# Kernel tuning notes

Measured on AMD Instinct MI355X. Metric: run time of the kernel, lower is better.

Reference implementation:

```python
import jax, jax.numpy as jnp
import numpy as np

B, H, S, D = 2, 16, 2048, 64

def setup_inputs() -> dict:
    key = jax.random.key(0)
    kq, kk, kv = jax.random.split(key, 3)
    Q = jax.random.normal(kq, (B, H, S, D), dtype=jnp.float32)
    K = jax.random.normal(kk, (B, H, S, D), dtype=jnp.float32)
    V = jax.random.normal(kv, (B, H, S, D), dtype=jnp.float32)
    return {"Q": Q, "K": K, "V": V}

def reference(Q, K, V):
    # scores: [B, H, S, S]
    scale = 1.0 / jnp.sqrt(jnp.asarray(Q.shape[-1], Q.dtype))
    scores = jnp.einsum('bhqd,bhkd->bhqk', Q, K) * scale
    probs = jax.nn.softmax(scores, axis=-1)
    out = jnp.einsum('bhqk,bhkd->bhqd', probs, V)
    return out
```

## Files before the change

kernel.cpp:

```cpp
#include <hip/hip_runtime.h>
#include <hip/hip_bf16.h>


#define Bn 2
#define Hn 16
#define Sn 2048
#define Dn 64
#define KP 72
#define OP 68

typedef __attribute__((ext_vector_type(8)))  short s16x8;
typedef __attribute__((ext_vector_type(16))) float f32x16;

__device__ __forceinline__ float fast_exp2(float x) {
#if __has_builtin(__builtin_amdgcn_exp2f)
    return __builtin_amdgcn_exp2f(x);
#else
    return exp2f(x);
#endif
}
__device__ __forceinline__ unsigned short f2bf(float f) {
    unsigned u = __float_as_uint(f);
    return (unsigned short)((u + 0x7fffu + ((u >> 16) & 1u)) >> 16);
}
__device__ __forceinline__ unsigned pack2bf(float lo, float hi) {
    return (unsigned)f2bf(lo) | ((unsigned)f2bf(hi) << 16);
}
__device__ __forceinline__ unsigned packtrunc(float lo, float hi) {
#if __has_builtin(__builtin_amdgcn_perm)
    return __builtin_amdgcn_perm(__float_as_uint(hi), __float_as_uint(lo),
                                 0x07060302u);
#else
    return (__float_as_uint(lo) >> 16) | (__float_as_uint(hi) & 0xffff0000u);
#endif
}
__device__ __forceinline__ s16x8 lds_frag(const unsigned short* p) {
    uint4 u = *(const uint4*)p;
    return __builtin_bit_cast(s16x8, u);
}
__device__ __forceinline__ s16x8 reg_frag(uint4 u) {
    return __builtin_bit_cast(s16x8, u);
}

__global__ __launch_bounds__(256)
void cast_kv2(const float* __restrict__ K, const float* __restrict__ V,
              unsigned short* __restrict__ Kb, unsigned short* __restrict__ Vt) {
    __shared__ unsigned short TK[64 * 72];
    __shared__ unsigned short TV[64 * 72];
    const int tid = threadIdx.x;
    const int bh  = blockIdx.x >> 5;
    const int kt  = blockIdx.x & 31;
    const int r = tid >> 2, cc = (tid & 3) * 16;

    const size_t rowbase = ((size_t)bh * Sn + (size_t)kt * 64 + r) * Dn + cc;
    {
        const float* ks = K + rowbase;
        #pragma unroll
        for (int i = 0; i < 2; ++i) {
            float4 f0 = *(const float4*)(ks + 8 * i);
            float4 f1 = *(const float4*)(ks + 8 * i + 4);
            uint4 w;
            w.x = pack2bf(f0.x, f0.y); w.y = pack2bf(f0.z, f0.w);
            w.z = pack2bf(f1.x, f1.y); w.w = pack2bf(f1.z, f1.w);
            *(uint4*)(TK + r * 72 + cc + 8 * i) = w;
        }
    }
    {
        const float* vs = V + rowbase;
        #pragma unroll
        for (int i = 0; i < 4; ++i) {
            float4 f = *(const float4*)(vs + 4 * i);
            const int d0 = cc + 4 * i;
            TV[(d0 + 0) * 72 + r] = f2bf(f.x);
            TV[(d0 + 1) * 72 + r] = f2bf(f.y);
            TV[(d0 + 2) * 72 + r] = f2bf(f.z);
            TV[(d0 + 3) * 72 + r] = f2bf(f.w);
        }
    }
    __syncthreads();
    unsigned short* kd = Kb + ((size_t)(bh * 32 + kt) * 8) * 512;
    unsigned short* vd = Vt + ((size_t)(bh * 32 + kt) * 8) * 512;
    #pragma unroll
    for (int i = 0; i < 2; ++i) {
        const int u = i * 256 + tid;
        const int c = u >> 6, lane = u & 63;
        const int l31 = lane & 31, hf = lane >> 5;
        const int sub = c >> 2, ks = c & 3;
        const int off = (sub * 32 + l31) * 72 + ks * 16 + hf * 8;
        *(uint4*)(kd + c * 512 + lane * 8) = *(const uint4*)(TK + off);
        *(uint4*)(vd + c * 512 + lane * 8) = *(const uint4*)(TV + off);
    }
}

__global__ __launch_bounds__(256, 4)
void attn_fwd_mfma5(const float* __restrict__ Q,
                    const unsigned short* __restrict__ Kb,
                    const unsigned short* __restrict__ Vt,
                    float* __restrict__ O) {
    __shared__ __align__(16) char smem[18432];
    unsigned short* PT = (unsigned short*)smem;
    float* ob = (float*)smem;
    float* lb = ob + 64 * OP;

    const int tid  = threadIdx.x;
    const int wave = tid >> 6;
    const int lane = tid & 63;
    const int l31  = lane & 31;
    const int half = lane >> 5;
    const int qg   = wave & 1;
    const int kh   = wave >> 1;

    const int bh = blockIdx.x & 31;
    const int q0 = (blockIdx.x >> 5) * 64;

    const float FCT = 0.18033688011112042f;

    s16x8 qf[4];
    {
        const float* qp = Q + ((size_t)bh * Sn + q0 + qg * 32 + l31) * Dn;
        #pragma unroll
        for (int ks = 0; ks < 4; ++ks) {
            const int d0 = ks * 16 + half * 8;
            float4 f0 = *(const float4*)(qp + d0);
            float4 f1 = *(const float4*)(qp + d0 + 4);
            uint4 u;
            u.x = pack2bf(f0.x * FCT, f0.y * FCT);
            u.y = pack2bf(f0.z * FCT, f0.w * FCT);
            u.z = pack2bf(f1.x * FCT, f1.y * FCT);
            u.w = pack2bf(f1.z * FCT, f1.w * FCT);
            qf[ks] = __builtin_bit_cast(s16x8, u);
        }
    }

    f32x16 acc0, acc1;
    #pragma unroll
    for (int r = 0; r < 16; ++r) { acc0[r] = 0.f; acc1[r] = 0.f; }
    float l = 0.f;

    const unsigned short* kbase =
        Kb + ((size_t)(bh * 32 + kh * 16) * 8) * 512 + (size_t)lane * 8;
    const unsigned short* vbase =
        Vt + ((size_t)(bh * 32 + kh * 16) * 8) * 512 + (size_t)lane * 8;

    unsigned short* ptw = PT + ((size_t)wave * 32 + l31) * KP;

    #pragma unroll 1
    for (int t = 0; t < 16; ++t) {
        uint4 kk[8];
        #pragma unroll
        for (int c = 0; c < 8; ++c)
            kk[c] = *(const uint4*)(kbase + (size_t)(t * 8 + c) * 512);

        f32x16 c0, c1;
        #pragma unroll
        for (int r = 0; r < 16; ++r) { c0[r] = 0.f; c1[r] = 0.f; }
        #pragma unroll
        for (int ks = 0; ks < 4; ++ks) {
            c0 = __builtin_amdgcn_mfma_f32_32x32x16_bf16(reg_frag(kk[ks]),     qf[ks], c0, 0, 0, 0);
            c1 = __builtin_amdgcn_mfma_f32_32x32x16_bf16(reg_frag(kk[4 + ks]), qf[ks], c1, 0, 0, 0);
        }

        uint4 vv[8];
        #pragma unroll
        for (int c = 0; c < 8; ++c)
            vv[c] = *(const uint4*)(vbase + (size_t)(t * 8 + c) * 512);

        #pragma unroll
        for (int r = 0; r < 16; ++r) {
            c0[r] = fast_exp2(c0[r]);
            c1[r] = fast_exp2(c1[r]);
        }
        float a0 = 0.f, a1 = 0.f, a2 = 0.f, a3 = 0.f;
        #pragma unroll
        for (int r = 0; r < 16; r += 4) {
            a0 += c0[r]     + c1[r];
            a1 += c0[r + 1] + c1[r + 1];
            a2 += c0[r + 2] + c1[r + 2];
            a3 += c0[r + 3] + c1[r + 3];
        }
        l += (a0 + a1) + (a2 + a3);

        #pragma unroll
        for (int g = 0; g < 4; ++g) {
            uint2 w0, w1;
            w0.x = packtrunc(c0[4 * g + 0], c0[4 * g + 1]);
            w0.y = packtrunc(c0[4 * g + 2], c0[4 * g + 3]);
            w1.x = packtrunc(c1[4 * g + 0], c1[4 * g + 1]);
            w1.y = packtrunc(c1[4 * g + 2], c1[4 * g + 3]);
            *(uint2*)(ptw + 8 * g + 4 * half)      = w0;
            *(uint2*)(ptw + 8 * g + 4 * half + 32) = w1;
        }

        #pragma unroll
        for (int ks = 0; ks < 4; ++ks) {
            s16x8 pf = lds_frag(ptw + ks * 16 + half * 8);
            acc0 = __builtin_amdgcn_mfma_f32_32x32x16_bf16(reg_frag(vv[ks]),     pf, acc0, 0, 0, 0);
            acc1 = __builtin_amdgcn_mfma_f32_32x32x16_bf16(reg_frag(vv[4 + ks]), pf, acc1, 0, 0, 0);
        }
    }

    l += __shfl_xor(l, 32, 64);

    __syncthreads();
    const int qrow = qg * 32 + l31;
    if (kh == 0) {
        #pragma unroll
        for (int g = 0; g < 4; ++g) {
            const int d0 = 8 * g + 4 * half;
            float4 f;
            f.x = acc0[4*g+0]; f.y = acc0[4*g+1]; f.z = acc0[4*g+2]; f.w = acc0[4*g+3];
            *(float4*)(ob + qrow * OP + d0) = f;
            f.x = acc1[4*g+0]; f.y = acc1[4*g+1]; f.z = acc1[4*g+2]; f.w = acc1[4*g+3];
            *(float4*)(ob + qrow * OP + d0 + 32) = f;
        }
        if (half == 0) lb[qrow] = l;
    }
    __syncthreads();
    if (kh == 1) {
        const float inv = 1.0f / (l + lb[qrow]);
        #pragma unroll
        for (int g = 0; g < 4; ++g) {
            const int d0 = 8 * g + 4 * half;
            float* p;
            float4 f;
            p = ob + qrow * OP + d0;        f = *(float4*)p;
            f.x = (f.x + acc0[4*g+0]) * inv; f.y = (f.y + acc0[4*g+1]) * inv;
            f.z = (f.z + acc0[4*g+2]) * inv; f.w = (f.w + acc0[4*g+3]) * inv;
            *(float4*)p = f;
            p = ob + qrow * OP + d0 + 32;   f = *(float4*)p;
            f.x = (f.x + acc1[4*g+0]) * inv; f.y = (f.y + acc1[4*g+1]) * inv;
            f.z = (f.z + acc1[4*g+2]) * inv; f.w = (f.w + acc1[4*g+3]) * inv;
            *(float4*)p = f;
        }
    }
    __syncthreads();
    float* op = O + ((size_t)bh * Sn + q0) * Dn;
    #pragma unroll
    for (int it = 0; it < 4; ++it) {
        const int idx = it * 256 + tid;
        const int r = idx >> 4, c4 = (idx & 15) * 4;
        *(float4*)(op + r * Dn + c4) = *(float4*)(ob + r * OP + c4);
    }
}

extern "C" void kernel_launch(void* const* d_in, const int* in_sizes, int n_in,
                              void* d_out, int out_size, void* d_ws, size_t ws_size,
                              hipStream_t stream) {
    const float* Q = (const float*)d_in[0];
    const float* K = (const float*)d_in[1];
    const float* V = (const float*)d_in[2];
    float* O = (float*)d_out;

    const size_t elems = (size_t)Bn * Hn * Sn * Dn;
    unsigned short* Kb = (unsigned short*)d_ws;
    unsigned short* Vt = Kb + elems;

    cast_kv2<<<dim3(Bn * Hn * (Sn / 64)), dim3(256), 0, stream>>>(K, V, Kb, Vt);
    attn_fwd_mfma5<<<dim3(Bn * Hn * (Sn / 64)), dim3(256), 0, stream>>>(Q, Kb, Vt, O);
}
```

Before: 139.8 us.

## Split key range four ways per block with 32-query tiles

Each block now handles 32 queries instead of 64, and all four waves share the same query rows while each takes a quarter of the key sequence. Partial outputs and row sums are merged serially through shared memory over several barriers. The grid doubles in size and launch bounds rise to allow more resident blocks, aiming for better CU fill and latency hiding. In exchange, each K/V tile is loaded by twice as many blocks, which doubles global/L2 traffic, and the reduction adds synchronization.

```diff
diff --git a/kernel.cpp b/kernel.cpp
--- a/kernel.cpp
+++ b/kernel.cpp
@@ -92,32 +92,30 @@
     }
 }
 
-__global__ __launch_bounds__(256, 4)
-void attn_fwd_mfma5(const float* __restrict__ Q,
+__global__ __launch_bounds__(256, 5)
+void attn_fwd_mfma6(const float* __restrict__ Q,
                     const unsigned short* __restrict__ Kb,
                     const unsigned short* __restrict__ Vt,
                     float* __restrict__ O) {
     __shared__ __align__(16) char smem[18432];
     unsigned short* PT = (unsigned short*)smem;
     float* ob = (float*)smem;
-    float* lb = ob + 64 * OP;
+    float* lb = ob + 32 * OP;
 
     const int tid  = threadIdx.x;
     const int wave = tid >> 6;
     const int lane = tid & 63;
     const int l31  = lane & 31;
     const int half = lane >> 5;
-    const int qg   = wave & 1;
-    const int kh   = wave >> 1;
 
     const int bh = blockIdx.x & 31;
-    const int q0 = (blockIdx.x >> 5) * 64;
+    const int q0 = (blockIdx.x >> 5) * 32;
 
     const float FCT = 0.18033688011112042f;
 
     s16x8 qf[4];
     {
-        const float* qp = Q + ((size_t)bh * Sn + q0 + qg * 32 + l31) * Dn;
+        const float* qp = Q + ((size_t)bh * Sn + q0 + l31) * Dn;
         #pragma unroll
         for (int ks = 0; ks < 4; ++ks) {
             const int d0 = ks * 16 + half * 8;
@@ -138,14 +136,14 @@
     float l = 0.f;
 
     const unsigned short* kbase =
-        Kb + ((size_t)(bh * 32 + kh * 16) * 8) * 512 + (size_t)lane * 8;
+        Kb + ((size_t)(bh * 32 + wave * 8) * 8) * 512 + (size_t)lane * 8;
     const unsigned short* vbase =
-        Vt + ((size_t)(bh * 32 + kh * 16) * 8) * 512 + (size_t)lane * 8;
+        Vt + ((size_t)(bh * 32 + wave * 8) * 8) * 512 + (size_t)lane * 8;
 
     unsigned short* ptw = PT + ((size_t)wave * 32 + l31) * KP;
 
     #pragma unroll 1
-    for (int t = 0; t < 16; ++t) {
+    for (int t = 0; t < 8; ++t) {
         uint4 kk[8];
         #pragma unroll
         for (int c = 0; c < 8; ++c)
@@ -202,32 +200,56 @@
     l += __shfl_xor(l, 32, 64);
 
     __syncthreads();
-    const int qrow = qg * 32 + l31;
-    if (kh == 0) {
+    if (wave == 0) {
         #pragma unroll
         for (int g = 0; g < 4; ++g) {
             const int d0 = 8 * g + 4 * half;
             float4 f;
             f.x = acc0[4*g+0]; f.y = acc0[4*g+1]; f.z = acc0[4*g+2]; f.w = acc0[4*g+3];
-            *(float4*)(ob + qrow * OP + d0) = f;
+            *(float4*)(ob + l31 * OP + d0) = f;
             f.x = acc1[4*g+0]; f.y = acc1[4*g+1]; f.z = acc1[4*g+2]; f.w = acc1[4*g+3];
-            *(float4*)(ob + qrow * OP + d0 + 32) = f;
-        }
-        if (half == 0) lb[qrow] = l;
-    }
-    __syncthreads();
-    if (kh == 1) {
-        const float inv = 1.0f / (l + lb[qrow]);
+            *(float4*)(ob + l31 * OP + d0 + 32) = f;
+        }
+        if (half == 0) lb[l31] = l;
+    }
+    __syncthreads();
+    if (wave == 1 || wave == 2) {
+        for (int w = 1; w <= 2; ++w) {
+            if (wave == w) {
+                #pragma unroll
+                for (int g = 0; g < 4; ++g) {
+                    const int d0 = 8 * g + 4 * half;
+                    float4 f;
+                    float* p;
+                    p = ob + l31 * OP + d0;       f = *(float4*)p;
+                    f.x += acc0[4*g+0]; f.y += acc0[4*g+1];
+                    f.z += acc0[4*g+2]; f.w += acc0[4*g+3];
+                    *(float4*)p = f;
+                    p = ob + l31 * OP + d0 + 32;  f = *(float4*)p;
+                    f.x += acc1[4*g+0]; f.y += acc1[4*g+1];
+                    f.z += acc1[4*g+2]; f.w += acc1[4*g+3];
+                    *(float4*)p = f;
+                }
+                if (half == 0) lb[l31] += l;
+            }
+            __syncthreads();
+        }
+    } else {
+        __syncthreads();
+        __syncthreads();
+    }
+    if (wave == 3) {
+        const float inv = 1.0f / (l + lb[l31]);
         #pragma unroll
         for (int g = 0; g < 4; ++g) {
             const int d0 = 8 * g + 4 * half;
+            float4 f;
             float* p;
-            float4 f;
-            p = ob + qrow * OP + d0;        f = *(float4*)p;
+            p = ob + l31 * OP + d0;       f = *(float4*)p;
             f.x = (f.x + acc0[4*g+0]) * inv; f.y = (f.y + acc0[4*g+1]) * inv;
             f.z = (f.z + acc0[4*g+2]) * inv; f.w = (f.w + acc0[4*g+3]) * inv;
             *(float4*)p = f;
-            p = ob + qrow * OP + d0 + 32;   f = *(float4*)p;
+            p = ob + l31 * OP + d0 + 32;  f = *(float4*)p;
             f.x = (f.x + acc1[4*g+0]) * inv; f.y = (f.y + acc1[4*g+1]) * inv;
             f.z = (f.z + acc1[4*g+2]) * inv; f.w = (f.w + acc1[4*g+3]) * inv;
             *(float4*)p = f;
@@ -236,7 +258,7 @@
     __syncthreads();
     float* op = O + ((size_t)bh * Sn + q0) * Dn;
     #pragma unroll
-    for (int it = 0; it < 4; ++it) {
+    for (int it = 0; it < 2; ++it) {
         const int idx = it * 256 + tid;
         const int r = idx >> 4, c4 = (idx & 15) * 4;
         *(float4*)(op + r * Dn + c4) = *(float4*)(ob + r * OP + c4);
@@ -256,5 +278,5 @@
     unsigned short* Vt = Kb + elems;
 
     cast_kv2<<<dim3(Bn * Hn * (Sn / 64)), dim3(256), 0, stream>>>(K, V, Kb, Vt);
-    attn_fwd_mfma5<<<dim3(Bn * Hn * (Sn / 64)), dim3(256), 0, stream>>>(Q, Kb, Vt, O);
-}
+    attn_fwd_mfma6<<<dim3(Bn * Hn * (Sn / 32)), dim3(256), 0, stream>>>(Q, Kb, Vt, O);
+}
```

Result: slower. 174.9 us (+25.2%).
